# Kernel optimization log

Measured on AMD Instinct MI355X. Metric: run time of the kernel, lower is better.

## Reference

```python
import jax, jax.numpy as jnp
import numpy as np

H = 64  # hidden_size

def _lstm_layer(x_tbi, h0, c0, w_ih, w_hh, b_ih, b_hh):
    """x_tbi: [T,B,I]; returns (out [T,B,H], h_n [B,H], c_n [B,H]).
    PyTorch gate order: i, f, g, o."""
    b = b_ih + b_hh  # [4H]
    # Precompute input projections for all timesteps at once (memory-friendly GEMM)
    xg = jnp.einsum('tbi,gi->tbg', x_tbi, w_ih) + b  # [T,B,4H]

    def step(carry, xg_t):
        h, c = carry
        gates = xg_t + h @ w_hh.T  # [B,4H]
        i, f, g, o = jnp.split(gates, 4, axis=-1)
        i = jax.nn.sigmoid(i)
        f = jax.nn.sigmoid(f)
        g = jnp.tanh(g)
        o = jax.nn.sigmoid(o)
        c = f * c + i * g
        h = o * jnp.tanh(c)
        return (h, c), h

    (h_n, c_n), out = jax.lax.scan(step, (h0, c0), xg)
    return out, h_n, c_n


def setup_inputs() -> dict:
    key = jax.random.key(0)
    B, T, I, O = 256, 1024, 128, 128
    ks = jax.random.split(key, 12)
    s_ih0 = 1.0 / np.sqrt(H)
    inp = {
        'x': jax.random.normal(ks[0], (B, T, I), dtype=jnp.float32),
        'h0': jnp.zeros((2, B, H), dtype=jnp.float32),
        'c0': jnp.zeros((2, B, H), dtype=jnp.float32),
        'w_ih0': jax.random.uniform(ks[1], (4 * H, I), jnp.float32, -s_ih0, s_ih0),
        'w_hh0': jax.random.uniform(ks[2], (4 * H, H), jnp.float32, -s_ih0, s_ih0),
        'b_ih0': jax.random.uniform(ks[3], (4 * H,), jnp.float32, -s_ih0, s_ih0),
        'b_hh0': jax.random.uniform(ks[4], (4 * H,), jnp.float32, -s_ih0, s_ih0),
        'w_ih1': jax.random.uniform(ks[5], (4 * H, H), jnp.float32, -s_ih0, s_ih0),
        'w_hh1': jax.random.uniform(ks[6], (4 * H, H), jnp.float32, -s_ih0, s_ih0),
        'b_ih1': jax.random.uniform(ks[7], (4 * H,), jnp.float32, -s_ih0, s_ih0),
        'b_hh1': jax.random.uniform(ks[8], (4 * H,), jnp.float32, -s_ih0, s_ih0),
        'w_fc': jax.random.uniform(ks[9], (O, H), jnp.float32, -s_ih0, s_ih0),
        'b_fc': jax.random.uniform(ks[10], (O,), jnp.float32, -s_ih0, s_ih0),
    }
    return inp


def reference(x, h0, c0, w_ih0, w_hh0, b_ih0, b_hh0, w_ih1, w_hh1, b_ih1, b_hh1, w_fc, b_fc):
    # x: [B,T,I] (batch_first) -> time-major [T,B,I]
    x_tbi = jnp.swapaxes(x, 0, 1)
    out0, h0n, c0n = _lstm_layer(x_tbi, h0[0], c0[0], w_ih0, w_hh0, b_ih0, b_hh0)
    # Dropout(p=0.5) between layers is identity in eval mode.
    out1, h1n, c1n = _lstm_layer(out0, h0[1], c0[1], w_ih1, w_hh1, b_ih1, b_hh1)
    out = jnp.swapaxes(out1, 0, 1)  # [B,T,H]
    flat = out.reshape(-1, H)  # [B*T, H]
    logits = flat @ w_fc.T + b_fc  # [B*T, O]
    h_n = jnp.stack([h0n, h1n], axis=0)  # [2,B,H]
    c_n = jnp.stack([c0n, c1n], axis=0)
    return logits, (h_n, c_n)
```

## Files before the change

kernel.cpp:

```cpp
#include <hip/hip_runtime.h>

#define T_STEPS 1024
#define HSZ     64
#define OSZ     128

typedef float4 F4;

__device__ __forceinline__ float fast_rcp(float x) { return __builtin_amdgcn_rcpf(x); }
__device__ __forceinline__ float tanh_fast(float x) {
    float e = __expf(2.0f * x);
    return fmaf(-2.0f, fast_rcp(e + 1.0f), 1.0f);
}

#define DOT(W, i) { F4 v_ = vs[i]; \
    a0 = fmaf(v_.x, (W).x, a0); a1 = fmaf(v_.y, (W).y, a1); \
    a2 = fmaf(v_.z, (W).z, a2); a3 = fmaf(v_.w, (W).w, a3); }

#define GATE_SELECT(act, gt, iv, fv, gv, ov) \
    float q1 = __shfl_xor((act), 1); \
    float q2 = __shfl_xor((act), 2); \
    float q3 = __shfl_xor((act), 3); \
    const bool b0 = (gt) & 1, b1 = (gt) & 2; \
    float iv = b1 ? (b0 ? q3 : q2) : (b0 ? q1 : (act)); \
    float fv = b1 ? (b0 ? q2 : q3) : (b0 ? (act) : q1); \
    float gv = b1 ? (b0 ? q1 : (act)) : (b0 ? q3 : q2); \
    float ov = b1 ? (b0 ? (act) : q1) : (b0 ? q2 : q3);

extern "C" __global__ void __launch_bounds__(512, 1)
lstm_l0(const float* __restrict__ x,
        const float* __restrict__ h0, const float* __restrict__ c0,
        const float* __restrict__ w_ih,
        const float* __restrict__ w_hh,
        const float* __restrict__ b_ih, const float* __restrict__ b_hh,
        float* __restrict__ out0,
        float* __restrict__ hn, float* __restrict__ cn)
{
    const int t_ = threadIdx.x;
    const int b  = blockIdx.x;
    const bool isScan = (t_ < 256);
    const int u  = t_ & 255;
    const int j  = u >> 2;
    const int gt = u & 3;

    __shared__ __align__(16) float xbuf[64 * 128];
    __shared__ __align__(16) float obuf[2][64 * HSZ];
    __shared__ __align__(16) float xg[2][4][65];
    __shared__ __align__(16) float hbuf[2][HSZ];

    F4 W00,W01,W02,W03,W04,W05,W06,W07,W08,W09,W10,W11,W12,W13,W14,W15;
    F4 W16,W17,W18,W19,W20,W21,W22,W23,W24,W25,W26,W27,W28,W29,W30,W31;
    {
        const F4 z = {0.f, 0.f, 0.f, 0.f};
        if (isScan) {
            const F4* ws = reinterpret_cast<const F4*>(w_hh + (size_t)(gt * HSZ + j) * HSZ);
            W00=ws[0]; W01=ws[1]; W02=ws[2];  W03=ws[3];  W04=ws[4];  W05=ws[5];  W06=ws[6];  W07=ws[7];
            W08=ws[8]; W09=ws[9]; W10=ws[10]; W11=ws[11]; W12=ws[12]; W13=ws[13]; W14=ws[14]; W15=ws[15];
            W16=z; W17=z; W18=z; W19=z; W20=z; W21=z; W22=z; W23=z;
            W24=z; W25=z; W26=z; W27=z; W28=z; W29=z; W30=z; W31=z;
        } else {
            const F4* ws = reinterpret_cast<const F4*>(w_ih + (size_t)u * 128);
            W00=ws[0];  W01=ws[1];  W02=ws[2];  W03=ws[3];  W04=ws[4];  W05=ws[5];  W06=ws[6];  W07=ws[7];
            W08=ws[8];  W09=ws[9];  W10=ws[10]; W11=ws[11]; W12=ws[12]; W13=ws[13]; W14=ws[14]; W15=ws[15];
            W16=ws[16]; W17=ws[17]; W18=ws[18]; W19=ws[19]; W20=ws[20]; W21=ws[21]; W22=ws[22]; W23=ws[23];
            W24=ws[24]; W25=ws[25]; W26=ws[26]; W27=ws[27]; W28=ws[28]; W29=ws[29]; W30=ws[30]; W31=ws[31];
        }
    }
    const float bias = isScan ? 0.f : (b_ih[u] + b_hh[u]);
    const float am = (gt == 2) ? -2.0f : -1.0f;
    const float aa = (gt == 2) ?  2.0f :  1.0f;
    const float ab = (gt == 2) ? -1.0f :  0.0f;

    float c = 0.f, h = 0.f;
    if (isScan) {
        c = c0[(size_t)b * HSZ + j];
        if (gt == 0) hbuf[0][j] = h0[(size_t)b * HSZ + j];
    }
    {
        const F4* src = reinterpret_cast<const F4*>(x + (size_t)b * T_STEPS * 128);
        F4* dst = reinterpret_cast<F4*>(xbuf);
        #pragma unroll
        for (int k = 0; k < 4; ++k) dst[t_ + 512 * k] = src[t_ + 512 * k];
    }
    __syncthreads();
    if (!isScan) {
        const F4* vs = reinterpret_cast<const F4*>(xbuf);
        float a0=0.f,a1=0.f,a2=0.f,a3=0.f;
        DOT(W00,0)  DOT(W01,1)  DOT(W02,2)  DOT(W03,3)  DOT(W04,4)  DOT(W05,5)  DOT(W06,6)  DOT(W07,7)
        DOT(W08,8)  DOT(W09,9)  DOT(W10,10) DOT(W11,11) DOT(W12,12) DOT(W13,13) DOT(W14,14) DOT(W15,15)
        DOT(W16,16) DOT(W17,17) DOT(W18,18) DOT(W19,19) DOT(W20,20) DOT(W21,21) DOT(W22,22) DOT(W23,23)
        DOT(W24,24) DOT(W25,25) DOT(W26,26) DOT(W27,27) DOT(W28,28) DOT(W29,29) DOT(W30,30) DOT(W31,31)
        xg[0][u >> 6][u & 63] = bias + (a0 + a1) + (a2 + a3);
    }
    __syncthreads();

    for (int t = 0; t < T_STEPS; ++t) {
        if (((t & 63) == 63) && t < 1023) {
            const F4* src = reinterpret_cast<const F4*>(x + ((size_t)b * T_STEPS + t + 1) * 128);
            F4* dst = reinterpret_cast<F4*>(xbuf);
            #pragma unroll
            for (int k = 0; k < 4; ++k) dst[t_ + 512 * k] = src[t_ + 512 * k];
            __syncthreads();
        }
        const int p = t & 1;
        if (isScan) {
            const F4* vs = reinterpret_cast<const F4*>(hbuf[p]);
            float a0=0.f,a1=0.f,a2=0.f,a3=0.f;
            DOT(W00,0)  DOT(W01,1)  DOT(W02,2)  DOT(W03,3)  DOT(W04,4)  DOT(W05,5)  DOT(W06,6)  DOT(W07,7)
            DOT(W08,8)  DOT(W09,9)  DOT(W10,10) DOT(W11,11) DOT(W12,12) DOT(W13,13) DOT(W14,14) DOT(W15,15)
            float pre = xg[p][gt][j] + (a0 + a1) + (a2 + a3);
            float act = fmaf(aa, fast_rcp(1.0f + __expf(am * pre)), ab);
            GATE_SELECT(act, gt, iv, fv, gv, ov)
            c = fmaf(fv, c, iv * gv);
            h = ov * tanh_fast(c);
            if (gt == 0) { hbuf[p ^ 1][j] = h; obuf[(t >> 6) & 1][(t & 63) * HSZ + j] = h; }
        } else {
            if (t < 1023) {
                const F4* vs = reinterpret_cast<const F4*>(xbuf + ((t + 1) & 63) * 128);
                float a0=0.f,a1=0.f,a2=0.f,a3=0.f;
                DOT(W00,0)  DOT(W01,1)  DOT(W02,2)  DOT(W03,3)  DOT(W04,4)  DOT(W05,5)  DOT(W06,6)  DOT(W07,7)
                DOT(W08,8)  DOT(W09,9)  DOT(W10,10) DOT(W11,11) DOT(W12,12) DOT(W13,13) DOT(W14,14) DOT(W15,15)
                DOT(W16,16) DOT(W17,17) DOT(W18,18) DOT(W19,19) DOT(W20,20) DOT(W21,21) DOT(W22,22) DOT(W23,23)
                DOT(W24,24) DOT(W25,25) DOT(W26,26) DOT(W27,27) DOT(W28,28) DOT(W29,29) DOT(W30,30) DOT(W31,31)
                xg[p ^ 1][u >> 6][u & 63] = bias + (a0 + a1) + (a2 + a3);
            }
            if ((t & 63) == 1 && t > 64) {
                const int cc = (t >> 6) - 1;
                const F4* s4 = reinterpret_cast<const F4*>(obuf[cc & 1]);
                F4* dst = reinterpret_cast<F4*>(out0 + ((size_t)b * T_STEPS + cc * 64) * HSZ);
                #pragma unroll
                for (int k = 0; k < 4; ++k) dst[u + 256 * k] = s4[u + 256 * k];
            }
        }
        __syncthreads();
    }
    {
        const F4* s4 = reinterpret_cast<const F4*>(obuf[1]);
        F4* dst = reinterpret_cast<F4*>(out0 + ((size_t)b * T_STEPS + 15 * 64) * HSZ);
        #pragma unroll
        for (int k = 0; k < 2; ++k) dst[t_ + 512 * k] = s4[t_ + 512 * k];
    }
    if (isScan && gt == 0) {
        hn[(size_t)b * HSZ + j] = h;
        cn[(size_t)b * HSZ + j] = c;
    }
}

extern "C" __global__ void __launch_bounds__(512, 1)
lstm_l1_fc(const float* __restrict__ in0,
           const float* __restrict__ h0, const float* __restrict__ c0,
           const float* __restrict__ w_ih,
           const float* __restrict__ w_hh,
           const float* __restrict__ b_ih, const float* __restrict__ b_hh,
           const float* __restrict__ w_fc,
           const float* __restrict__ b_fc,
           float* __restrict__ logits,
           float* __restrict__ hn, float* __restrict__ cn)
{
    const int t_ = threadIdx.x;
    const int b  = blockIdx.x;
    const bool isScan = (t_ < 256);
    const int u  = t_ & 255;
    const int j  = u >> 2;
    const int gt = u & 3;
    const int o  = u >> 1;
    const int hh = u & 1;

    __shared__ __align__(16) float ibuf[64 * HSZ];
    __shared__ __align__(16) float lbuf[2][64 * OSZ];
    __shared__ __align__(16) float xg[2][4][65];
    __shared__ __align__(16) float hbuf[2][HSZ];

    F4 W00,W01,W02,W03,W04,W05,W06,W07,W08,W09,W10,W11,W12,W13,W14,W15;
    F4 W16,W17,W18,W19,W20,W21,W22,W23;
    {
        if (isScan) {
            const F4 z = {0.f, 0.f, 0.f, 0.f};
            const F4* ws = reinterpret_cast<const F4*>(w_hh + (size_t)(gt * HSZ + j) * HSZ);
            W00=ws[0]; W01=ws[1]; W02=ws[2];  W03=ws[3];  W04=ws[4];  W05=ws[5];  W06=ws[6];  W07=ws[7];
            W08=ws[8]; W09=ws[9]; W10=ws[10]; W11=ws[11]; W12=ws[12]; W13=ws[13]; W14=ws[14]; W15=ws[15];
            W16=z; W17=z; W18=z; W19=z; W20=z; W21=z; W22=z; W23=z;
        } else {
            const F4* ws = reinterpret_cast<const F4*>(w_ih + (size_t)u * HSZ);
            W00=ws[0]; W01=ws[1]; W02=ws[2];  W03=ws[3];  W04=ws[4];  W05=ws[5];  W06=ws[6];  W07=ws[7];
            W08=ws[8]; W09=ws[9]; W10=ws[10]; W11=ws[11]; W12=ws[12]; W13=ws[13]; W14=ws[14]; W15=ws[15];
            const F4* wf = reinterpret_cast<const F4*>(w_fc + (size_t)o * HSZ + hh * 32);
            W16=wf[0]; W17=wf[1]; W18=wf[2]; W19=wf[3]; W20=wf[4]; W21=wf[5]; W22=wf[6]; W23=wf[7];
        }
    }
    const float bias = isScan ? 0.f : (b_ih[u] + b_hh[u]);
    const float bfc  = b_fc[o];
    const float am = (gt == 2) ? -2.0f : -1.0f;
    const float aa = (gt == 2) ?  2.0f :  1.0f;
    const float ab = (gt == 2) ? -1.0f :  0.0f;

    float c = 0.f, h = 0.f;
    if (isScan) {
        c = c0[(size_t)b * HSZ + j];
        if (gt == 0) hbuf[0][j] = h0[(size_t)b * HSZ + j];
    }
    {
        const F4* src = reinterpret_cast<const F4*>(in0 + (size_t)b * T_STEPS * HSZ);
        F4* dst = reinterpret_cast<F4*>(ibuf);
        #pragma unroll
        for (int k = 0; k < 2; ++k) dst[t_ + 512 * k] = src[t_ + 512 * k];
    }
    __syncthreads();
    if (!isScan) {
        const F4* vs = reinterpret_cast<const F4*>(ibuf);
        float a0=0.f,a1=0.f,a2=0.f,a3=0.f;
        DOT(W00,0)  DOT(W01,1)  DOT(W02,2)  DOT(W03,3)  DOT(W04,4)  DOT(W05,5)  DOT(W06,6)  DOT(W07,7)
        DOT(W08,8)  DOT(W09,9)  DOT(W10,10) DOT(W11,11) DOT(W12,12) DOT(W13,13) DOT(W14,14) DOT(W15,15)
        xg[0][u >> 6][u & 63] = bias + (a0 + a1) + (a2 + a3);
    }
    __syncthreads();

    for (int t = 0; t < T_STEPS; ++t) {
        if (((t & 63) == 63) && t < 1023) {
            const F4* src = reinterpret_cast<const F4*>(in0 + ((size_t)b * T_STEPS + t + 1) * HSZ);
            F4* dst = reinterpret_cast<F4*>(ibuf);
            #pragma unroll
            for (int k = 0; k < 2; ++k) dst[t_ + 512 * k] = src[t_ + 512 * k];
            __syncthreads();
        }
        const int p = t & 1;
        if (isScan) {
            const F4* vs = reinterpret_cast<const F4*>(hbuf[p]);
            float a0=0.f,a1=0.f,a2=0.f,a3=0.f;
            DOT(W00,0)  DOT(W01,1)  DOT(W02,2)  DOT(W03,3)  DOT(W04,4)  DOT(W05,5)  DOT(W06,6)  DOT(W07,7)
            DOT(W08,8)  DOT(W09,9)  DOT(W10,10) DOT(W11,11) DOT(W12,12) DOT(W13,13) DOT(W14,14) DOT(W15,15)
            float pre = xg[p][gt][j] + (a0 + a1) + (a2 + a3);
            float act = fmaf(aa, fast_rcp(1.0f + __expf(am * pre)), ab);
            GATE_SELECT(act, gt, iv, fv, gv, ov)
            c = fmaf(fv, c, iv * gv);
            h = ov * tanh_fast(c);
            if (gt == 0) hbuf[p ^ 1][j] = h;
        } else {
            if (t < 1023) {
                const F4* vs = reinterpret_cast<const F4*>(ibuf + ((t + 1) & 63) * HSZ);
                float a0=0.f,a1=0.f,a2=0.f,a3=0.f;
                DOT(W00,0)  DOT(W01,1)  DOT(W02,2)  DOT(W03,3)  DOT(W04,4)  DOT(W05,5)  DOT(W06,6)  DOT(W07,7)
                DOT(W08,8)  DOT(W09,9)  DOT(W10,10) DOT(W11,11) DOT(W12,12) DOT(W13,13) DOT(W14,14) DOT(W15,15)
                xg[p ^ 1][u >> 6][u & 63] = bias + (a0 + a1) + (a2 + a3);
            }
            if (t > 0) {
                const F4* vs = reinterpret_cast<const F4*>(&hbuf[p][hh * 32]);
                float a0=0.f,a1=0.f,a2=0.f,a3=0.f;
                DOT(W16,0) DOT(W17,1) DOT(W18,2) DOT(W19,3) DOT(W20,4) DOT(W21,5) DOT(W22,6) DOT(W23,7)
                float f = (a0 + a1) + (a2 + a3);
                f += __shfl_xor(f, 1);
                if (hh == 0) lbuf[((t - 1) >> 6) & 1][((t - 1) & 63) * OSZ + o] = f + bfc;
            }
            if ((t & 63) == 1 && t > 64) {
                const int cc = (t >> 6) - 1;
                const F4* s4 = reinterpret_cast<const F4*>(lbuf[cc & 1]);
                F4* dst = reinterpret_cast<F4*>(logits + ((size_t)b * T_STEPS + cc * 64) * OSZ);
                #pragma unroll
                for (int k = 0; k < 8; ++k) dst[u + 256 * k] = s4[u + 256 * k];
            }
        }
        __syncthreads();
    }
    if (!isScan) {
        const F4* vs = reinterpret_cast<const F4*>(&hbuf[0][hh * 32]);
        float a0=0.f,a1=0.f,a2=0.f,a3=0.f;
        DOT(W16,0) DOT(W17,1) DOT(W18,2) DOT(W19,3) DOT(W20,4) DOT(W21,5) DOT(W22,6) DOT(W23,7)
        float f = (a0 + a1) + (a2 + a3);
        f += __shfl_xor(f, 1);
        if (hh == 0) lbuf[1][63 * OSZ + o] = f + bfc;
    }
    __syncthreads();
    {
        const F4* s4 = reinterpret_cast<const F4*>(lbuf[1]);
        F4* dst = reinterpret_cast<F4*>(logits + ((size_t)b * T_STEPS + 15 * 64) * OSZ);
        #pragma unroll
        for (int k = 0; k < 4; ++k) dst[t_ + 512 * k] = s4[t_ + 512 * k];
    }
    if (isScan && gt == 0) {
        hn[(size_t)b * HSZ + j] = h;
        cn[(size_t)b * HSZ + j] = c;
    }
}

extern "C" void kernel_launch(void* const* d_in, const int* in_sizes, int n_in,
                              void* d_out, int out_size, void* d_ws, size_t ws_size,
                              hipStream_t stream) {
    const float* x     = (const float*)d_in[0];
    const float* h0    = (const float*)d_in[1];
    const float* c0    = (const float*)d_in[2];
    const float* w_ih0 = (const float*)d_in[3];
    const float* w_hh0 = (const float*)d_in[4];
    const float* b_ih0 = (const float*)d_in[5];
    const float* b_hh0 = (const float*)d_in[6];
    const float* w_ih1 = (const float*)d_in[7];
    const float* w_hh1 = (const float*)d_in[8];
    const float* b_ih1 = (const float*)d_in[9];
    const float* b_hh1 = (const float*)d_in[10];
    const float* w_fc  = (const float*)d_in[11];
    const float* b_fc  = (const float*)d_in[12];

    float* out = (float*)d_out;
    const size_t n_logits = (size_t)256 * T_STEPS * OSZ;
    const size_t n_state  = (size_t)256 * HSZ;
    float* logits = out;
    float* hn     = out + n_logits;
    float* cn     = hn + 2 * n_state;

    float* out0 = (float*)d_ws;

    lstm_l0<<<256, 512, 0, stream>>>(
        x, h0, c0, w_ih0, w_hh0, b_ih0, b_hh0, out0, hn, cn);

    lstm_l1_fc<<<256, 512, 0, stream>>>(
        out0, h0 + n_state, c0 + n_state,
        w_ih1, w_hh1, b_ih1, b_hh1, w_fc, b_fc,
        logits, hn + n_state, cn + n_state);
}
```

Baseline: 1.894 ms.

## Replace producer/consumer warp split with chunked projection then serial scan

The two kernels drop the 512-thread layout, where half the threads computed input projections one timestep ahead of the scan threads. Each 256-thread block now computes the input projection for 64 timesteps as a register-tiled batch GEMM into shared memory, then runs 64 serial scan steps. In layer 1 the FC output is also done per chunk as a batched GEMM, written straight to global memory. This removes the per-step projection work and half-empty warps from the critical path, but the projection phase is no longer overlapped with the scan and the recurrent weights have to be reloaded after each chunk.

```diff
diff --git a/kernel.cpp b/kernel.cpp
--- a/kernel.cpp
+++ b/kernel.cpp
@@ -11,10 +11,6 @@
     float e = __expf(2.0f * x);
     return fmaf(-2.0f, fast_rcp(e + 1.0f), 1.0f);
 }
-
-#define DOT(W, i) { F4 v_ = vs[i]; \
-    a0 = fmaf(v_.x, (W).x, a0); a1 = fmaf(v_.y, (W).y, a1); \
-    a2 = fmaf(v_.z, (W).z, a2); a3 = fmaf(v_.w, (W).w, a3); }
 
 #define GATE_SELECT(act, gt, iv, fv, gv, ov) \
     float q1 = __shfl_xor((act), 1); \
@@ -26,7 +22,92 @@
     float gv = b1 ? (b0 ? q1 : (act)) : (b0 ? q3 : q2); \
     float ov = b1 ? (b0 ? (act) : q1) : (b0 ? q2 : q3);
 
-extern "C" __global__ void __launch_bounds__(512, 1)
+struct WHH { F4 w[16]; };
+
+__device__ __forceinline__ WHH load_whh(const F4* base) {
+    WHH W;
+    #pragma unroll
+    for (int k = 0; k < 16; ++k) W.w[k] = base[k];
+    return W;
+}
+
+__device__ __forceinline__ void proj128(const F4* wih4 , const F4* xb4,
+                                        float* xgb, int u, float gbias) {
+    #pragma unroll 1
+    for (int pass = 0; pass < 2; ++pass) {
+        const int s0 = pass * 32;
+        float acc[32];
+        #pragma unroll
+        for (int s = 0; s < 32; ++s) acc[s] = gbias;
+        #pragma unroll 4
+        for (int kb = 0; kb < 16; ++kb) {
+            F4 w0 = wih4[kb * 2], w1 = wih4[kb * 2 + 1];
+            #pragma unroll
+            for (int s = 0; s < 32; ++s) {
+                F4 x0 = xb4[(s0 + s) * 32 + kb * 2];
+                F4 x1 = xb4[(s0 + s) * 32 + kb * 2 + 1];
+                acc[s] = fmaf(x0.x, w0.x, acc[s]); acc[s] = fmaf(x0.y, w0.y, acc[s]);
+                acc[s] = fmaf(x0.z, w0.z, acc[s]); acc[s] = fmaf(x0.w, w0.w, acc[s]);
+                acc[s] = fmaf(x1.x, w1.x, acc[s]); acc[s] = fmaf(x1.y, w1.y, acc[s]);
+                acc[s] = fmaf(x1.z, w1.z, acc[s]); acc[s] = fmaf(x1.w, w1.w, acc[s]);
+            }
+        }
+        #pragma unroll
+        for (int s = 0; s < 32; ++s) xgb[(s0 + s) * 256 + u] = acc[s];
+    }
+}
+
+__device__ __forceinline__ void proj64(const F4* wih4 , const F4* xb4,
+                                       float* xgb, int u, float gbias) {
+    #pragma unroll 1
+    for (int pass = 0; pass < 2; ++pass) {
+        const int s0 = pass * 32;
+        float acc[32];
+        #pragma unroll
+        for (int s = 0; s < 32; ++s) acc[s] = gbias;
+        #pragma unroll 4
+        for (int kb = 0; kb < 8; ++kb) {
+            F4 w0 = wih4[kb * 2], w1 = wih4[kb * 2 + 1];
+            #pragma unroll
+            for (int s = 0; s < 32; ++s) {
+                F4 x0 = xb4[(s0 + s) * 16 + kb * 2];
+                F4 x1 = xb4[(s0 + s) * 16 + kb * 2 + 1];
+                acc[s] = fmaf(x0.x, w0.x, acc[s]); acc[s] = fmaf(x0.y, w0.y, acc[s]);
+                acc[s] = fmaf(x0.z, w0.z, acc[s]); acc[s] = fmaf(x0.w, w0.w, acc[s]);
+                acc[s] = fmaf(x1.x, w1.x, acc[s]); acc[s] = fmaf(x1.y, w1.y, acc[s]);
+                acc[s] = fmaf(x1.z, w1.z, acc[s]); acc[s] = fmaf(x1.w, w1.w, acc[s]);
+            }
+        }
+        #pragma unroll
+        for (int s = 0; s < 32; ++s) xgb[(s0 + s) * 256 + u] = acc[s];
+    }
+}
+
+__device__ __forceinline__ void scan_chunk(const WHH& W, const float* xgb, float (*hbuf)[HSZ],
+                                           float* obuf, int tglob0, int u, int j, int gt,
+                                           float am, float aa, float ab, float& c, float& h) {
+    #pragma unroll 1
+    for (int tc = 0; tc < 64; ++tc) {
+        const int p = (tglob0 + tc) & 1;
+        const F4* hv = reinterpret_cast<const F4*>(hbuf[p]);
+        float a0 = 0.f, a1 = 0.f, a2 = 0.f, a3 = 0.f;
+        #pragma unroll
+        for (int k = 0; k < 16; ++k) {
+            F4 v = hv[k];
+            a0 = fmaf(v.x, W.w[k].x, a0); a1 = fmaf(v.y, W.w[k].y, a1);
+            a2 = fmaf(v.z, W.w[k].z, a2); a3 = fmaf(v.w, W.w[k].w, a3);
+        }
+        float pre = xgb[tc * 256 + gt * HSZ + j] + (a0 + a1) + (a2 + a3);
+        float act = fmaf(aa, fast_rcp(1.0f + __expf(am * pre)), ab);
+        GATE_SELECT(act, gt, iv, fv, gv, ov)
+        c = fmaf(fv, c, iv * gv);
+        h = ov * tanh_fast(c);
+        if (gt == 0) { hbuf[p ^ 1][j] = h; obuf[tc * HSZ + j] = h; }
+        __syncthreads();
+    }
+}
+
+extern "C" __global__ void __launch_bounds__(256)
 lstm_l0(const float* __restrict__ x,
         const float* __restrict__ h0, const float* __restrict__ c0,
         const float* __restrict__ w_ih,
@@ -35,247 +116,158 @@
         float* __restrict__ out0,
         float* __restrict__ hn, float* __restrict__ cn)
 {
-    const int t_ = threadIdx.x;
-    const int b  = blockIdx.x;
-    const bool isScan = (t_ < 256);
-    const int u  = t_ & 255;
-    const int j  = u >> 2;
-    const int gt = u & 3;
+    const int u = threadIdx.x, b = blockIdx.x;
+    const int j = u >> 2, gt = u & 3;
 
     __shared__ __align__(16) float xbuf[64 * 128];
-    __shared__ __align__(16) float obuf[2][64 * HSZ];
-    __shared__ __align__(16) float xg[2][4][65];
+    __shared__ __align__(16) float xgb[64 * 256];
+    __shared__ __align__(16) float obuf[64 * HSZ];
     __shared__ __align__(16) float hbuf[2][HSZ];
 
-    F4 W00,W01,W02,W03,W04,W05,W06,W07,W08,W09,W10,W11,W12,W13,W14,W15;
-    F4 W16,W17,W18,W19,W20,W21,W22,W23,W24,W25,W26,W27,W28,W29,W30,W31;
-    {
-        const F4 z = {0.f, 0.f, 0.f, 0.f};
-        if (isScan) {
-            const F4* ws = reinterpret_cast<const F4*>(w_hh + (size_t)(gt * HSZ + j) * HSZ);
-            W00=ws[0]; W01=ws[1]; W02=ws[2];  W03=ws[3];  W04=ws[4];  W05=ws[5];  W06=ws[6];  W07=ws[7];
-            W08=ws[8]; W09=ws[9]; W10=ws[10]; W11=ws[11]; W12=ws[12]; W13=ws[13]; W14=ws[14]; W15=ws[15];
-            W16=z; W17=z; W18=z; W19=z; W20=z; W21=z; W22=z; W23=z;
-            W24=z; W25=z; W26=z; W27=z; W28=z; W29=z; W30=z; W31=z;
-        } else {
-            const F4* ws = reinterpret_cast<const F4*>(w_ih + (size_t)u * 128);
-            W00=ws[0];  W01=ws[1];  W02=ws[2];  W03=ws[3];  W04=ws[4];  W05=ws[5];  W06=ws[6];  W07=ws[7];
-            W08=ws[8];  W09=ws[9];  W10=ws[10]; W11=ws[11]; W12=ws[12]; W13=ws[13]; W14=ws[14]; W15=ws[15];
-            W16=ws[16]; W17=ws[17]; W18=ws[18]; W19=ws[19]; W20=ws[20]; W21=ws[21]; W22=ws[22]; W23=ws[23];
-            W24=ws[24]; W25=ws[25]; W26=ws[26]; W27=ws[27]; W28=ws[28]; W29=ws[29]; W30=ws[30]; W31=ws[31];
-        }
-    }
-    const float bias = isScan ? 0.f : (b_ih[u] + b_hh[u]);
+    const float gbias = b_ih[u] + b_hh[u];
     const float am = (gt == 2) ? -2.0f : -1.0f;
     const float aa = (gt == 2) ?  2.0f :  1.0f;
     const float ab = (gt == 2) ? -1.0f :  0.0f;
 
-    float c = 0.f, h = 0.f;
-    if (isScan) {
-        c = c0[(size_t)b * HSZ + j];
-        if (gt == 0) hbuf[0][j] = h0[(size_t)b * HSZ + j];
-    }
+    const F4* wih4 = reinterpret_cast<const F4*>(w_ih) + (size_t)u * 32;
+    const F4* whh4 = reinterpret_cast<const F4*>(w_hh) + (size_t)(gt * HSZ + j) * 16;
+    const F4* xb4  = reinterpret_cast<const F4*>(xbuf);
+
+    float c = c0[(size_t)b * HSZ + j];
+    float h = 0.f;
+    if (gt == 0) hbuf[0][j] = h0[(size_t)b * HSZ + j];
+
     {
         const F4* src = reinterpret_cast<const F4*>(x + (size_t)b * T_STEPS * 128);
         F4* dst = reinterpret_cast<F4*>(xbuf);
         #pragma unroll
-        for (int k = 0; k < 4; ++k) dst[t_ + 512 * k] = src[t_ + 512 * k];
+        for (int k = 0; k < 8; ++k) dst[u + 256 * k] = src[u + 256 * k];
     }
     __syncthreads();
-    if (!isScan) {
-        const F4* vs = reinterpret_cast<const F4*>(xbuf);
-        float a0=0.f,a1=0.f,a2=0.f,a3=0.f;
-        DOT(W00,0)  DOT(W01,1)  DOT(W02,2)  DOT(W03,3)  DOT(W04,4)  DOT(W05,5)  DOT(W06,6)  DOT(W07,7)
-        DOT(W08,8)  DOT(W09,9)  DOT(W10,10) DOT(W11,11) DOT(W12,12) DOT(W13,13) DOT(W14,14) DOT(W15,15)
-        DOT(W16,16) DOT(W17,17) DOT(W18,18) DOT(W19,19) DOT(W20,20) DOT(W21,21) DOT(W22,22) DOT(W23,23)
-        DOT(W24,24) DOT(W25,25) DOT(W26,26) DOT(W27,27) DOT(W28,28) DOT(W29,29) DOT(W30,30) DOT(W31,31)
-        xg[0][u >> 6][u & 63] = bias + (a0 + a1) + (a2 + a3);
-    }
+    proj128(wih4, xb4, xgb, u, gbias);
     __syncthreads();
-
-    for (int t = 0; t < T_STEPS; ++t) {
-        if (((t & 63) == 63) && t < 1023) {
-            const F4* src = reinterpret_cast<const F4*>(x + ((size_t)b * T_STEPS + t + 1) * 128);
+    WHH W = load_whh(whh4);
+
+    #pragma unroll 1
+    for (int ch = 0; ch < 16; ++ch) {
+        if (ch < 15) {
+            const F4* src = reinterpret_cast<const F4*>(x + ((size_t)b * T_STEPS + (ch + 1) * 64) * 128);
             F4* dst = reinterpret_cast<F4*>(xbuf);
             #pragma unroll
-            for (int k = 0; k < 4; ++k) dst[t_ + 512 * k] = src[t_ + 512 * k];
-            __syncthreads();
-        }
-        const int p = t & 1;
-        if (isScan) {
-            const F4* vs = reinterpret_cast<const F4*>(hbuf[p]);
-            float a0=0.f,a1=0.f,a2=0.f,a3=0.f;
-            DOT(W00,0)  DOT(W01,1)  DOT(W02,2)  DOT(W03,3)  DOT(W04,4)  DOT(W05,5)  DOT(W06,6)  DOT(W07,7)
-            DOT(W08,8)  DOT(W09,9)  DOT(W10,10) DOT(W11,11) DOT(W12,12) DOT(W13,13) DOT(W14,14) DOT(W15,15)
-            float pre = xg[p][gt][j] + (a0 + a1) + (a2 + a3);
-            float act = fmaf(aa, fast_rcp(1.0f + __expf(am * pre)), ab);
-            GATE_SELECT(act, gt, iv, fv, gv, ov)
-            c = fmaf(fv, c, iv * gv);
-            h = ov * tanh_fast(c);
-            if (gt == 0) { hbuf[p ^ 1][j] = h; obuf[(t >> 6) & 1][(t & 63) * HSZ + j] = h; }
-        } else {
-            if (t < 1023) {
-                const F4* vs = reinterpret_cast<const F4*>(xbuf + ((t + 1) & 63) * 128);
-                float a0=0.f,a1=0.f,a2=0.f,a3=0.f;
-                DOT(W00,0)  DOT(W01,1)  DOT(W02,2)  DOT(W03,3)  DOT(W04,4)  DOT(W05,5)  DOT(W06,6)  DOT(W07,7)
-                DOT(W08,8)  DOT(W09,9)  DOT(W10,10) DOT(W11,11) DOT(W12,12) DOT(W13,13) DOT(W14,14) DOT(W15,15)
-                DOT(W16,16) DOT(W17,17) DOT(W18,18) DOT(W19,19) DOT(W20,20) DOT(W21,21) DOT(W22,22) DOT(W23,23)
-                DOT(W24,24) DOT(W25,25) DOT(W26,26) DOT(W27,27) DOT(W28,28) DOT(W29,29) DOT(W30,30) DOT(W31,31)
-                xg[p ^ 1][u >> 6][u & 63] = bias + (a0 + a1) + (a2 + a3);
-            }
-            if ((t & 63) == 1 && t > 64) {
-                const int cc = (t >> 6) - 1;
-                const F4* s4 = reinterpret_cast<const F4*>(obuf[cc & 1]);
-                F4* dst = reinterpret_cast<F4*>(out0 + ((size_t)b * T_STEPS + cc * 64) * HSZ);
-                #pragma unroll
-                for (int k = 0; k < 4; ++k) dst[u + 256 * k] = s4[u + 256 * k];
-            }
-        }
-        __syncthreads();
-    }
-    {
-        const F4* s4 = reinterpret_cast<const F4*>(obuf[1]);
-        F4* dst = reinterpret_cast<F4*>(out0 + ((size_t)b * T_STEPS + 15 * 64) * HSZ);
-        #pragma unroll
-        for (int k = 0; k < 2; ++k) dst[t_ + 512 * k] = s4[t_ + 512 * k];
-    }
-    if (isScan && gt == 0) {
+            for (int k = 0; k < 8; ++k) dst[u + 256 * k] = src[u + 256 * k];
+        }
+        __syncthreads();
+
+        scan_chunk(W, xgb, hbuf, obuf, ch * 64, u, j, gt, am, aa, ab, c, h);
+
+        {
+            const F4* s4 = reinterpret_cast<const F4*>(obuf);
+            F4* dst = reinterpret_cast<F4*>(out0 + ((size_t)b * T_STEPS + ch * 64) * HSZ);
+            #pragma unroll
+            for (int k = 0; k < 4; ++k) dst[u + 256 * k] = s4[u + 256 * k];
+        }
+        if (ch < 15) {
+            proj128(wih4, xb4, xgb, u, gbias);
+            W = load_whh(whh4);
+        }
+        __syncthreads();
+    }
+
+    if (gt == 0) {
         hn[(size_t)b * HSZ + j] = h;
         cn[(size_t)b * HSZ + j] = c;
     }
 }
 
-extern "C" __global__ void __launch_bounds__(512, 1)
-lstm_l1_fc(const float* __restrict__ in0,
-           const float* __restrict__ h0, const float* __restrict__ c0,
-           const float* __restrict__ w_ih,
-           const float* __restrict__ w_hh,
-           const float* __restrict__ b_ih, const float* __restrict__ b_hh,
-           const float* __restrict__ w_fc,
-           const float* __restrict__ b_fc,
-           float* __restrict__ logits,
-           float* __restrict__ hn, float* __restrict__ cn)
+extern "C" __global__ void __launch_bounds__(256)
+lstm_l1(const float* __restrict__ in0,
+        const float* __restrict__ h0, const float* __restrict__ c0,
+        const float* __restrict__ w_ih,
+        const float* __restrict__ w_hh,
+        const float* __restrict__ b_ih, const float* __restrict__ b_hh,
+        const float* __restrict__ w_fc,
+        const float* __restrict__ b_fc,
+        float* __restrict__ logits,
+        float* __restrict__ hn, float* __restrict__ cn)
 {
-    const int t_ = threadIdx.x;
-    const int b  = blockIdx.x;
-    const bool isScan = (t_ < 256);
-    const int u  = t_ & 255;
-    const int j  = u >> 2;
-    const int gt = u & 3;
-    const int o  = u >> 1;
-    const int hh = u & 1;
-
-    __shared__ __align__(16) float ibuf[64 * HSZ];
-    __shared__ __align__(16) float lbuf[2][64 * OSZ];
-    __shared__ __align__(16) float xg[2][4][65];
+    const int u = threadIdx.x, b = blockIdx.x;
+    const int j = u >> 2, gt = u & 3;
+    const int o = u & 127, th = u >> 7;
+
+    __shared__ __align__(16) float xbuf[64 * HSZ];
+    __shared__ __align__(16) float xgb[64 * 256];
+    __shared__ __align__(16) float obuf[64 * HSZ];
     __shared__ __align__(16) float hbuf[2][HSZ];
 
-    F4 W00,W01,W02,W03,W04,W05,W06,W07,W08,W09,W10,W11,W12,W13,W14,W15;
-    F4 W16,W17,W18,W19,W20,W21,W22,W23;
-    {
-        if (isScan) {
-            const F4 z = {0.f, 0.f, 0.f, 0.f};
-            const F4* ws = reinterpret_cast<const F4*>(w_hh + (size_t)(gt * HSZ + j) * HSZ);
-            W00=ws[0]; W01=ws[1]; W02=ws[2];  W03=ws[3];  W04=ws[4];  W05=ws[5];  W06=ws[6];  W07=ws[7];
-            W08=ws[8]; W09=ws[9]; W10=ws[10]; W11=ws[11]; W12=ws[12]; W13=ws[13]; W14=ws[14]; W15=ws[15];
-            W16=z; W17=z; W18=z; W19=z; W20=z; W21=z; W22=z; W23=z;
-        } else {
-            const F4* ws = reinterpret_cast<const F4*>(w_ih + (size_t)u * HSZ);
-            W00=ws[0]; W01=ws[1]; W02=ws[2];  W03=ws[3];  W04=ws[4];  W05=ws[5];  W06=ws[6];  W07=ws[7];
-            W08=ws[8]; W09=ws[9]; W10=ws[10]; W11=ws[11]; W12=ws[12]; W13=ws[13]; W14=ws[14]; W15=ws[15];
-            const F4* wf = reinterpret_cast<const F4*>(w_fc + (size_t)o * HSZ + hh * 32);
-            W16=wf[0]; W17=wf[1]; W18=wf[2]; W19=wf[3]; W20=wf[4]; W21=wf[5]; W22=wf[6]; W23=wf[7];
-        }
-    }
-    const float bias = isScan ? 0.f : (b_ih[u] + b_hh[u]);
-    const float bfc  = b_fc[o];
+    const float gbias = b_ih[u] + b_hh[u];
+    const float bfc   = b_fc[o];
     const float am = (gt == 2) ? -2.0f : -1.0f;
     const float aa = (gt == 2) ?  2.0f :  1.0f;
     const float ab = (gt == 2) ? -1.0f :  0.0f;
 
-    float c = 0.f, h = 0.f;
-    if (isScan) {
-        c = c0[(size_t)b * HSZ + j];
-        if (gt == 0) hbuf[0][j] = h0[(size_t)b * HSZ + j];
-    }
+    const F4* wih4 = reinterpret_cast<const F4*>(w_ih) + (size_t)u * 16;
+    const F4* whh4 = reinterpret_cast<const F4*>(w_hh) + (size_t)(gt * HSZ + j) * 16;
+    const F4* wfc4 = reinterpret_cast<const F4*>(w_fc) + (size_t)o * 16;
+    const F4* xb4  = reinterpret_cast<const F4*>(xbuf);
+    const F4* ob4  = reinterpret_cast<const F4*>(obuf);
+
+    float c = c0[(size_t)b * HSZ + j];
+    float h = 0.f;
+    if (gt == 0) hbuf[0][j] = h0[(size_t)b * HSZ + j];
+
     {
         const F4* src = reinterpret_cast<const F4*>(in0 + (size_t)b * T_STEPS * HSZ);
-        F4* dst = reinterpret_cast<F4*>(ibuf);
-        #pragma unroll
-        for (int k = 0; k < 2; ++k) dst[t_ + 512 * k] = src[t_ + 512 * k];
+        F4* dst = reinterpret_cast<F4*>(xbuf);
+        #pragma unroll
+        for (int k = 0; k < 4; ++k) dst[u + 256 * k] = src[u + 256 * k];
     }
     __syncthreads();
-    if (!isScan) {
-        const F4* vs = reinterpret_cast<const F4*>(ibuf);
-        float a0=0.f,a1=0.f,a2=0.f,a3=0.f;
-        DOT(W00,0)  DOT(W01,1)  DOT(W02,2)  DOT(W03,3)  DOT(W04,4)  DOT(W05,5)  DOT(W06,6)  DOT(W07,7)
-        DOT(W08,8)  DOT(W09,9)  DOT(W10,10) DOT(W11,11) DOT(W12,12) DOT(W13,13) DOT(W14,14) DOT(W15,15)
-        xg[0][u >> 6][u & 63] = bias + (a0 + a1) + (a2 + a3);
-    }
+    proj64(wih4, xb4, xgb, u, gbias);
     __syncthreads();
-
-    for (int t = 0; t < T_STEPS; ++t) {
-        if (((t & 63) == 63) && t < 1023) {
-            const F4* src = reinterpret_cast<const F4*>(in0 + ((size_t)b * T_STEPS + t + 1) * HSZ);
-            F4* dst = reinterpret_cast<F4*>(ibuf);
-            #pragma unroll
-            for (int k = 0; k < 2; ++k) dst[t_ + 512 * k] = src[t_ + 512 * k];
-            __syncthreads();
-        }
-        const int p = t & 1;
-        if (isScan) {
-            const F4* vs = reinterpret_cast<const F4*>(hbuf[p]);
-            float a0=0.f,a1=0.f,a2=0.f,a3=0.f;
-            DOT(W00,0)  DOT(W01,1)  DOT(W02,2)  DOT(W03,3)  DOT(W04,4)  DOT(W05,5)  DOT(W06,6)  DOT(W07,7)
-            DOT(W08,8)  DOT(W09,9)  DOT(W10,10) DOT(W11,11) DOT(W12,12) DOT(W13,13) DOT(W14,14) DOT(W15,15)
-            float pre = xg[p][gt][j] + (a0 + a1) + (a2 + a3);
-            float act = fmaf(aa, fast_rcp(1.0f + __expf(am * pre)), ab);
-            GATE_SELECT(act, gt, iv, fv, gv, ov)
-            c = fmaf(fv, c, iv * gv);
-            h = ov * tanh_fast(c);
-            if (gt == 0) hbuf[p ^ 1][j] = h;
-        } else {
-            if (t < 1023) {
-                const F4* vs = reinterpret_cast<const F4*>(ibuf + ((t + 1) & 63) * HSZ);
-                float a0=0.f,a1=0.f,a2=0.f,a3=0.f;
-                DOT(W00,0)  DOT(W01,1)  DOT(W02,2)  DOT(W03,3)  DOT(W04,4)  DOT(W05,5)  DOT(W06,6)  DOT(W07,7)
-                DOT(W08,8)  DOT(W09,9)  DOT(W10,10) DOT(W11,11) DOT(W12,12) DOT(W13,13) DOT(W14,14) DOT(W15,15)
-                xg[p ^ 1][u >> 6][u & 63] = bias + (a0 + a1) + (a2 + a3);
+    WHH W = load_whh(whh4);
+
+    #pragma unroll 1
+    for (int ch = 0; ch < 16; ++ch) {
+        if (ch < 15) {
+            const F4* src = reinterpret_cast<const F4*>(in0 + ((size_t)b * T_STEPS + (ch + 1) * 64) * HSZ);
+            F4* dst = reinterpret_cast<F4*>(xbuf);
+            #pragma unroll
+            for (int k = 0; k < 4; ++k) dst[u + 256 * k] = src[u + 256 * k];
+        }
+        __syncthreads();
+
+        scan_chunk(W, xgb, hbuf, obuf, ch * 64, u, j, gt, am, aa, ab, c, h);
+
+        {
+            float fac[32];
+            #pragma unroll
+            for (int s = 0; s < 32; ++s) fac[s] = bfc;
+            #pragma unroll 4
+            for (int kb = 0; kb < 8; ++kb) {
+                F4 f0 = wfc4[kb * 2], f1 = wfc4[kb * 2 + 1];
+                #pragma unroll
+                for (int s = 0; s < 32; ++s) {
+                    F4 h0v = ob4[(th * 32 + s) * 16 + kb * 2];
+                    F4 h1v = ob4[(th * 32 + s) * 16 + kb * 2 + 1];
+                    fac[s] = fmaf(h0v.x, f0.x, fac[s]); fac[s] = fmaf(h0v.y, f0.y, fac[s]);
+                    fac[s] = fmaf(h0v.z, f0.z, fac[s]); fac[s] = fmaf(h0v.w, f0.w, fac[s]);
+                    fac[s] = fmaf(h1v.x, f1.x, fac[s]); fac[s] = fmaf(h1v.y, f1.y, fac[s]);
+                    fac[s] = fmaf(h1v.z, f1.z, fac[s]); fac[s] = fmaf(h1v.w, f1.w, fac[s]);
+                }
             }
-            if (t > 0) {
-                const F4* vs = reinterpret_cast<const F4*>(&hbuf[p][hh * 32]);
-                float a0=0.f,a1=0.f,a2=0.f,a3=0.f;
-                DOT(W16,0) DOT(W17,1) DOT(W18,2) DOT(W19,3) DOT(W20,4) DOT(W21,5) DOT(W22,6) DOT(W23,7)
-                float f = (a0 + a1) + (a2 + a3);
-                f += __shfl_xor(f, 1);
-                if (hh == 0) lbuf[((t - 1) >> 6) & 1][((t - 1) & 63) * OSZ + o] = f + bfc;
-            }
-            if ((t & 63) == 1 && t > 64) {
-                const int cc = (t >> 6) - 1;
-                const F4* s4 = reinterpret_cast<const F4*>(lbuf[cc & 1]);
-                F4* dst = reinterpret_cast<F4*>(logits + ((size_t)b * T_STEPS + cc * 64) * OSZ);
-                #pragma unroll
-                for (int k = 0; k < 8; ++k) dst[u + 256 * k] = s4[u + 256 * k];
-            }
-        }
-        __syncthreads();
-    }
-    if (!isScan) {
-        const F4* vs = reinterpret_cast<const F4*>(&hbuf[0][hh * 32]);
-        float a0=0.f,a1=0.f,a2=0.f,a3=0.f;
-        DOT(W16,0) DOT(W17,1) DOT(W18,2) DOT(W19,3) DOT(W20,4) DOT(W21,5) DOT(W22,6) DOT(W23,7)
-        float f = (a0 + a1) + (a2 + a3);
-        f += __shfl_xor(f, 1);
-        if (hh == 0) lbuf[1][63 * OSZ + o] = f + bfc;
-    }
-    __syncthreads();
-    {
-        const F4* s4 = reinterpret_cast<const F4*>(lbuf[1]);
-        F4* dst = reinterpret_cast<F4*>(logits + ((size_t)b * T_STEPS + 15 * 64) * OSZ);
-        #pragma unroll
-        for (int k = 0; k < 4; ++k) dst[t_ + 512 * k] = s4[t_ + 512 * k];
-    }
-    if (isScan && gt == 0) {
+            #pragma unroll
+            for (int s = 0; s < 32; ++s)
+                logits[((size_t)b * T_STEPS + ch * 64 + th * 32 + s) * OSZ + o] = fac[s];
+        }
+
+        if (ch < 15) {
+            proj64(wih4, xb4, xgb, u, gbias);
+            W = load_whh(whh4);
+        }
+        __syncthreads();
+    }
+
+    if (gt == 0) {
         hn[(size_t)b * HSZ + j] = h;
         cn[(size_t)b * HSZ + j] = c;
     }
@@ -307,10 +299,10 @@
 
     float* out0 = (float*)d_ws;
 
-    lstm_l0<<<256, 512, 0, stream>>>(
+    lstm_l0<<<256, 256, 0, stream>>>(
         x, h0, c0, w_ih0, w_hh0, b_ih0, b_hh0, out0, hn, cn);
 
-    lstm_l1_fc<<<256, 512, 0, stream>>>(
+    lstm_l1<<<256, 256, 0, stream>>>(
         out0, h0 + n_state, c0 + n_state,
         w_ih1, w_hh1, b_ih1, b_hh1, w_fc, b_fc,
         logits, hn + n_state, cn + n_state);
```

Measured after the change: 2.381 ms. 25.7% more time.
